# Optimization experiments

Hardware: AMD Instinct MI355X
Metric: run time of the kernel (lower is better)

The kernel has to match this reference:

```python
import jax, jax.numpy as jnp
import numpy as np

ALPHA = 2.0  # init kwarg alpha


def _edt(mask):
    """Exact Euclidean distance from each pixel to the nearest False pixel.
    mask: (H, W) bool. Matches scipy.ndimage.distance_transform_edt(mask).
    Separable algorithm: 1D L1 pass along columns, then exact min over columns.
    """
    H, W = mask.shape
    INF = jnp.float32(H + W)
    g0 = jnp.where(mask, INF, 0.0).astype(jnp.float32)  # 0 at background pixels

    def step(carry, row):
        g = jnp.minimum(row, carry + 1.0)
        return g, g

    _, fwd = jax.lax.scan(step, jnp.full((W,), INF, jnp.float32), g0)
    _, bwd = jax.lax.scan(step, jnp.full((W,), INF, jnp.float32), fwd[::-1])
    g = bwd[::-1]  # (H, W): vertical distance to nearest bg in same column

    j = jnp.arange(W, dtype=jnp.float32)
    d2 = (j[:, None] - j[None, :]) ** 2  # (Wj, Wk)
    # dist2[i, j] = min_k g[i, k]^2 + (j - k)^2   -> exact squared EDT
    dist2 = jnp.min(g[:, None, :] ** 2 + d2[None, :, :], axis=-1)  # (H, W)
    return jnp.sqrt(dist2)


def _distance_field(img):
    """img: (N, H, W) float. Replicates LogHausdorffDTLoss.distance_field per slice."""

    def one(ch):
        mask = ch > 0.5
        valid = jnp.logical_and(mask.any(), ~mask.all())
        field = _edt(mask) + _edt(~mask)  # fg_dist + bg_dist
        return jnp.where(valid, field, 0.0)

    # sequential map keeps peak memory to one (H, W, W) intermediate at a time
    return jax.lax.map(one, img)


def setup_inputs() -> dict:
    key = jax.random.key(0)
    k1, k2, k3 = jax.random.split(key, 3)
    B, C, H, W = 8, 4, 256, 256
    preds_S = jax.random.normal(k1, (B, C, H, W), dtype=jnp.float32)
    preds_T = jax.random.normal(k2, (B, C, H, W), dtype=jnp.float32)
    target = jax.random.uniform(k3, (B, 1, H, W), dtype=jnp.float32)
    return {"preds_S": preds_S, "preds_T": preds_T, "target": target}


def reference(preds_S, preds_T, target):
    # shapes already match -> no interpolation; sigmoid=False, softmax=True, C>1
    C = preds_S.shape[1]
    p = jax.nn.softmax(preds_S, axis=1)

    # to_onehot_y=True: target is overwritten by onehot(argmax(teacher)) (detached)
    pT = jax.lax.stop_gradient(preds_T)
    labels = jnp.argmax(pT, axis=1)  # (B, H, W)
    tgt = jax.nn.one_hot(labels, C, axis=1, dtype=p.dtype)  # (B, C, H, W)

    # include_background=False: drop channel 0
    p = p[:, 1:]
    tgt = tgt[:, 1:]
    B, Cc, H, W = p.shape

    pred_dt = _distance_field(jax.lax.stop_gradient(p).reshape(-1, H, W)).reshape(B, Cc, H, W)
    tgt_dt = _distance_field(tgt.reshape(-1, H, W)).reshape(B, Cc, H, W)
    pred_dt = jax.lax.stop_gradient(pred_dt)
    tgt_dt = jax.lax.stop_gradient(tgt_dt)

    err = (p - tgt) ** 2
    dist = pred_dt ** ALPHA + tgt_dt ** ALPHA
    # per-channel means all cover B*H*W elements -> mean of means == global mean
    loss = jnp.mean(err * dist)
    return jnp.log(loss + 1.0)
```

## Files before the change

### kernel.cpp

```cpp
#include <hip/hip_runtime.h>
#include <math.h>

#define HWTOT 65536
#define WD 256
#define HT 256
#define NSL 24

static constexpr size_t OFF_CNT   = 0;
static constexpr size_t OFF_PART  = 256;
static constexpr size_t HDR_BYTES = 256 + 6144 * 4;
static constexpr size_t OFF_MASK  = 24832;
static constexpr size_t OFF_ERR   = OFF_MASK + (size_t)NSL * HWTOT;
static constexpr size_t OFF_G     = OFF_ERR + (size_t)NSL * HWTOT * 2;

__global__ __launch_bounds__(256) void k_mask(
    const float* __restrict__ pS, const float* __restrict__ pT,
    unsigned char* __restrict__ mask, _Float16* __restrict__ err,
    int* __restrict__ cnts)
{
    __shared__ int lc[6];
    if (threadIdx.x < 6) lc[threadIdx.x] = 0;
    __syncthreads();

    int t  = blockIdx.x * 256 + threadIdx.x;
    int b  = t >> 16;
    int hw = t & (HWTOT - 1);

    const float* ps = pS + (size_t)b * 4 * HWTOT + hw;
    float s0 = ps[0], s1 = ps[HWTOT], s2 = ps[2 * HWTOT], s3 = ps[3 * HWTOT];
    float mx = fmaxf(fmaxf(s0, s1), fmaxf(s2, s3));
    float e0 = expf(s0 - mx), e1 = expf(s1 - mx), e2 = expf(s2 - mx), e3 = expf(s3 - mx);
    float inv = 1.0f / (e0 + e1 + e2 + e3);

    const float* pt = pT + (size_t)b * 4 * HWTOT + hw;
    float t0 = pt[0], t1 = pt[HWTOT], t2 = pt[2 * HWTOT], t3 = pt[3 * HWTOT];
    int lab = 0; float bm = t0;
    if (t1 > bm) { bm = t1; lab = 1; }
    if (t2 > bm) { bm = t2; lab = 2; }
    if (t3 > bm) { bm = t3; lab = 3; }

    float pv[3] = { e1 * inv, e2 * inv, e3 * inv };
    #pragma unroll
    for (int cc = 0; cc < 3; ++cc) {
        int sl = b * 3 + cc;
        bool mp = pv[cc] > 0.5f;
        bool mt = (lab == cc + 1);
        mask[(size_t)sl * HWTOT + hw] = (unsigned char)((mp ? 1 : 0) | (mt ? 2 : 0));
        float tcv = mt ? 1.0f : 0.0f;
        float ev = (pv[cc] - tcv) * (pv[cc] - tcv);
        err[(size_t)sl * HWTOT + hw] = (_Float16)ev;
        unsigned long long balP = __ballot(mp);
        unsigned long long balT = __ballot(mt);
        if ((threadIdx.x & 63) == 0) {
            atomicAdd(&lc[cc],     (int)__popcll(balP));
            atomicAdd(&lc[3 + cc], (int)__popcll(balT));
        }
    }
    __syncthreads();
    if (threadIdx.x < 3) {
        atomicAdd(&cnts[b * 3 + threadIdx.x], lc[threadIdx.x]);
    } else if (threadIdx.x < 6) {
        atomicAdd(&cnts[24 + b * 3 + (threadIdx.x - 3)], lc[threadIdx.x]);
    }
}

__global__ __launch_bounds__(256) void k_vert(
    const unsigned char* __restrict__ mask, unsigned short* __restrict__ g)
{
    int s = blockIdx.x;
    int f = blockIdx.y;
    int w = threadIdx.x;
    int bit = f >> 1;
    int pol = f & 1;

    const unsigned char* m = mask + (size_t)s * HWTOT + w;
    unsigned short* go = g + ((size_t)f * NSL + s) * HWTOT + w;

    unsigned gp[128];
    int prev = 512;
    #pragma unroll
    for (int hb = 0; hb < 16; ++hb) {
        unsigned char mb[16];
        #pragma unroll
        for (int i = 0; i < 16; ++i) mb[i] = m[(hb * 16 + i) * WD];
        #pragma unroll
        for (int i = 0; i < 16; ++i) {
            int h = hb * 16 + i;
            int mv = (mb[i] >> bit) & 1;
            int gv = (mv == pol) ? 0 : min(prev + 1, 512);
            prev = gv;
            if ((h & 1) == 0) gp[h >> 1] = (unsigned)gv;
            else              gp[h >> 1] |= (unsigned)gv << 16;
        }
    }
    prev = 512;
    #pragma unroll
    for (int hb = 15; hb >= 0; --hb) {
        unsigned short outv[16];
        #pragma unroll
        for (int i = 15; i >= 0; --i) {
            int h = hb * 16 + i;
            unsigned pk = gp[h >> 1];
            int gf = (h & 1) ? (int)(pk >> 16) : (int)(pk & 0xffffu);
            int gv = min(gf, prev + 1);
            prev = gv;
            outv[i] = (unsigned short)gv;
        }
        #pragma unroll
        for (int i = 0; i < 16; ++i) go[(hb * 16 + i) * WD] = outv[i];
    }
}

__global__ __launch_bounds__(256) void k_row(
    const _Float16* __restrict__ err, const unsigned short* __restrict__ gAll,
    const int* __restrict__ cnts, float* __restrict__ partials)
{
    int h  = blockIdx.x;
    int s  = blockIdx.y;
    int jo = threadIdx.x;

    __shared__ float4 g2[768];
    __shared__ float  wred[4];

    const size_t fstride = (size_t)NSL * HWTOT;
    size_t rbase = (size_t)s * HWTOT + h * WD + jo;

    int a  = gAll[rbase];
    int bb = gAll[fstride + rbase];
    int c  = gAll[2 * fstride + rbase];
    int dd = gAll[3 * fstride + rbase];

    int cp = cnts[s];
    int ct = cnts[24 + s];
    bool validP = (cp > 0) && (cp < HWTOT);
    bool validT = (ct > 0) && (ct < HWTOT);
    bool selP = (a > 0);
    bool selT = (c > 0);

    int gsp = selP ? a : bb; if (!validP) gsp = 0;
    int gst = selT ? c : dd; if (!validT) gst = 0;

    float fa = (float)(a * a), fb = (float)(bb * bb);
    float fc = (float)(c * c), fd = (float)(dd * dd);
    g2[256 + jo] = make_float4(fa, fb, fc, fd);
    float4 inf4 = make_float4(1e30f, 1e30f, 1e30f, 1e30f);
    g2[jo] = inf4;
    g2[512 + jo] = inf4;

    int R = min(max(gsp, gst), 256);
    #pragma unroll
    for (int i = 1; i < 64; i <<= 1) R = max(R, __shfl_xor(R, i));

    float m1 = (float)(gsp * gsp);
    float m2 = (float)(gst * gst);
    __syncthreads();

    for (int d = 1; d < R; ++d) {
        float4 L = g2[256 + jo - d];
        float4 Rv = g2[256 + jo + d];
        float d2 = (float)(d * d);
        float c1 = fminf(selP ? L.x : L.y, selP ? Rv.x : Rv.y);
        float c2 = fminf(selT ? L.z : L.w, selT ? Rv.z : Rv.w);
        m1 = fminf(m1, c1 + d2);
        m2 = fminf(m2, c2 + d2);
    }

    float contrib = (float)err[rbase] * (m1 + m2);

    #pragma unroll
    for (int off = 32; off > 0; off >>= 1) contrib += __shfl_down(contrib, off);
    if ((jo & 63) == 0) wred[jo >> 6] = contrib;
    __syncthreads();
    if (jo == 0) partials[s * 256 + h] = wred[0] + wred[1] + wred[2] + wred[3];
}

__global__ __launch_bounds__(256) void k_final(
    const float* __restrict__ partials, float* __restrict__ out)
{
    __shared__ double red[256];
    int t = threadIdx.x;
    double acc = 0.0;
    for (int i = t; i < NSL * 256; i += 256) acc += (double)partials[i];
    red[t] = acc;
    __syncthreads();
    for (int off = 128; off > 0; off >>= 1) {
        if (t < off) red[t] += red[t + off];
        __syncthreads();
    }
    if (t == 0) {
        double loss = red[0] / (double)((size_t)NSL * HWTOT);
        out[0] = (float)log(loss + 1.0);
    }
}

extern "C" void kernel_launch(void* const* d_in, const int* in_sizes, int n_in,
                              void* d_out, int out_size, void* d_ws, size_t ws_size,
                              hipStream_t stream)
{
    const float* pS = (const float*)d_in[0];
    const float* pT = (const float*)d_in[1];
    float* out = (float*)d_out;

    char* ws = (char*)d_ws;
    int*            cnts  = (int*)(ws + OFF_CNT);
    float*          parts = (float*)(ws + OFF_PART);
    unsigned char*  mask  = (unsigned char*)(ws + OFF_MASK);
    _Float16*       err   = (_Float16*)(ws + OFF_ERR);
    unsigned short* gAll  = (unsigned short*)(ws + OFF_G);

    hipMemsetAsync(ws, 0, HDR_BYTES, stream);

    k_mask <<<dim3(2048),     dim3(256), 0, stream>>>(pS, pT, mask, err, cnts);
    k_vert <<<dim3(NSL, 4),   dim3(256), 0, stream>>>(mask, gAll);
    k_row  <<<dim3(256, NSL), dim3(256), 0, stream>>>(err, gAll, cnts, parts);
    k_final<<<dim3(1),        dim3(256), 0, stream>>>(parts, out);
}
```

Before: 130.2 us.

## Compute combined boundary distance in one vertical pass and drop memset/atomics

```diff
diff --git a/kernel.cpp b/kernel.cpp
--- a/kernel.cpp
+++ b/kernel.cpp
@@ -6,25 +6,26 @@
 #define HT 256
 #define NSL 24
 
-static constexpr size_t OFF_CNT   = 0;
-static constexpr size_t OFF_PART  = 256;
-static constexpr size_t HDR_BYTES = 256 + 6144 * 4;
-static constexpr size_t OFF_MASK  = 24832;
-static constexpr size_t OFF_ERR   = OFF_MASK + (size_t)NSL * HWTOT;
-static constexpr size_t OFF_G     = OFF_ERR + (size_t)NSL * HWTOT * 2;
+static constexpr size_t OFF_CNT  = 0;
+static constexpr size_t OFF_PART = 256;
+static constexpr size_t OFF_PCNT = 24832;
+static constexpr size_t OFF_MASK = 49408;
+static constexpr size_t OFF_ERR  = OFF_MASK + (size_t)NSL * HWTOT;
+static constexpr size_t OFF_G    = OFF_ERR + (size_t)NSL * HWTOT * 2;
 
 __global__ __launch_bounds__(256) void k_mask(
     const float* __restrict__ pS, const float* __restrict__ pT,
     unsigned char* __restrict__ mask, _Float16* __restrict__ err,
-    int* __restrict__ cnts)
+    unsigned short* __restrict__ pcnt)
 {
     __shared__ int lc[6];
     if (threadIdx.x < 6) lc[threadIdx.x] = 0;
     __syncthreads();
 
-    int t  = blockIdx.x * 256 + threadIdx.x;
-    int b  = t >> 16;
-    int hw = t & (HWTOT - 1);
+    int blk = blockIdx.x;
+    int b   = blk >> 8;
+    int lb  = blk & 255;
+    int hw  = lb * 256 + threadIdx.x;
 
     const float* ps = pS + (size_t)b * 4 * HWTOT + hw;
     float s0 = ps[0], s1 = ps[HWTOT], s2 = ps[2 * HWTOT], s3 = ps[3 * HWTOT];
@@ -58,61 +59,75 @@
     }
     __syncthreads();
     if (threadIdx.x < 3) {
-        atomicAdd(&cnts[b * 3 + threadIdx.x], lc[threadIdx.x]);
+        int sl = b * 3 + threadIdx.x;
+        pcnt[(size_t)sl * 256 + lb] = (unsigned short)lc[threadIdx.x];
     } else if (threadIdx.x < 6) {
-        atomicAdd(&cnts[24 + b * 3 + (threadIdx.x - 3)], lc[threadIdx.x]);
-    }
-}
-
-__global__ __launch_bounds__(256) void k_vert(
-    const unsigned char* __restrict__ mask, unsigned short* __restrict__ g)
+        int sl = b * 3 + (threadIdx.x - 3);
+        pcnt[(size_t)(NSL + sl) * 256 + lb] = (unsigned short)lc[threadIdx.x];
+    }
+}
+
+__global__ __launch_bounds__(256, 1) void k_vert(
+    const unsigned char* __restrict__ mask, const unsigned short* __restrict__ pcnt,
+    unsigned short* __restrict__ g, int* __restrict__ cnts)
 {
     int s = blockIdx.x;
     int f = blockIdx.y;
     int w = threadIdx.x;
-    int bit = f >> 1;
-    int pol = f & 1;
 
     const unsigned char* m = mask + (size_t)s * HWTOT + w;
     unsigned short* go = g + ((size_t)f * NSL + s) * HWTOT + w;
 
-    unsigned gp[128];
-    int prev = 512;
+    unsigned up[128];
+    unsigned mb32[8];
+    int prevm = -1, d = 512;
     #pragma unroll
     for (int hb = 0; hb < 16; ++hb) {
-        unsigned char mb[16];
-        #pragma unroll
-        for (int i = 0; i < 16; ++i) mb[i] = m[(hb * 16 + i) * WD];
+        unsigned char mraw[16];
+        #pragma unroll
+        for (int i = 0; i < 16; ++i) mraw[i] = m[(hb * 16 + i) * WD];
         #pragma unroll
         for (int i = 0; i < 16; ++i) {
             int h = hb * 16 + i;
-            int mv = (mb[i] >> bit) & 1;
-            int gv = (mv == pol) ? 0 : min(prev + 1, 512);
-            prev = gv;
-            if ((h & 1) == 0) gp[h >> 1] = (unsigned)gv;
-            else              gp[h >> 1] |= (unsigned)gv << 16;
+            int mv = (mraw[i] >> f) & 1;
+            d = (prevm < 0) ? 512 : ((mv != prevm) ? 1 : min(d + 1, 512));
+            prevm = mv;
+            if (h & 1) up[h >> 1] |= (unsigned)d << 16;
+            else       up[h >> 1]  = (unsigned)d;
+            if ((h & 31) == 0) mb32[h >> 5]  = (unsigned)mv;
+            else               mb32[h >> 5] |= (unsigned)mv << (h & 31);
         }
     }
-    prev = 512;
+    int nextm = -1; d = 512;
     #pragma unroll
     for (int hb = 15; hb >= 0; --hb) {
         unsigned short outv[16];
         #pragma unroll
         for (int i = 15; i >= 0; --i) {
             int h = hb * 16 + i;
-            unsigned pk = gp[h >> 1];
-            int gf = (h & 1) ? (int)(pk >> 16) : (int)(pk & 0xffffu);
-            int gv = min(gf, prev + 1);
-            prev = gv;
-            outv[i] = (unsigned short)gv;
+            int mv = (mb32[h >> 5] >> (h & 31)) & 1;
+            d = (nextm < 0) ? 512 : ((mv != nextm) ? 1 : min(d + 1, 512));
+            nextm = mv;
+            unsigned pk = up[h >> 1];
+            int du = (h & 1) ? (int)(pk >> 16) : (int)(pk & 0xffffu);
+            outv[i] = (unsigned short)min(du, d);
         }
         #pragma unroll
         for (int i = 0; i < 16; ++i) go[(hb * 16 + i) * WD] = outv[i];
     }
+
+    __shared__ int cr[4];
+    int v = (int)pcnt[((size_t)f * NSL + s) * 256 + w];
+    #pragma unroll
+    for (int i = 1; i < 64; i <<= 1) v += __shfl_xor(v, i);
+    if ((w & 63) == 0) cr[w >> 6] = v;
+    __syncthreads();
+    if (w == 0) cnts[f * NSL + s] = cr[0] + cr[1] + cr[2] + cr[3];
 }
 
 __global__ __launch_bounds__(256) void k_row(
     const _Float16* __restrict__ err, const unsigned short* __restrict__ gAll,
+    const unsigned char* __restrict__ mask,
     const int* __restrict__ cnts, float* __restrict__ partials)
 {
     int h  = blockIdx.x;
@@ -125,28 +140,27 @@
     const size_t fstride = (size_t)NSL * HWTOT;
     size_t rbase = (size_t)s * HWTOT + h * WD + jo;
 
-    int a  = gAll[rbase];
-    int bb = gAll[fstride + rbase];
-    int c  = gAll[2 * fstride + rbase];
-    int dd = gAll[3 * fstride + rbase];
+    int gcP = gAll[rbase];
+    int gcT = gAll[fstride + rbase];
+    int mb  = mask[rbase];
+    bool selP = mb & 1;
+    bool selT = (mb >> 1) & 1;
 
     int cp = cnts[s];
-    int ct = cnts[24 + s];
+    int ct = cnts[NSL + s];
     bool validP = (cp > 0) && (cp < HWTOT);
     bool validT = (ct > 0) && (ct < HWTOT);
-    bool selP = (a > 0);
-    bool selT = (c > 0);
-
-    int gsp = selP ? a : bb; if (!validP) gsp = 0;
-    int gst = selT ? c : dd; if (!validT) gst = 0;
-
-    float fa = (float)(a * a), fb = (float)(bb * bb);
-    float fc = (float)(c * c), fd = (float)(dd * dd);
-    g2[256 + jo] = make_float4(fa, fb, fc, fd);
+
+    float fP = (float)(gcP * gcP);
+    float fT = (float)(gcT * gcT);
+    g2[256 + jo] = make_float4(selP ? fP : 0.0f, selP ? 0.0f : fP,
+                               selT ? fT : 0.0f, selT ? 0.0f : fT);
     float4 inf4 = make_float4(1e30f, 1e30f, 1e30f, 1e30f);
     g2[jo] = inf4;
     g2[512 + jo] = inf4;
 
+    int gsp = validP ? gcP : 0;
+    int gst = validT ? gcT : 0;
     int R = min(max(gsp, gst), 256);
     #pragma unroll
     for (int i = 1; i < 64; i <<= 1) R = max(R, __shfl_xor(R, i));
@@ -155,10 +169,10 @@
     float m2 = (float)(gst * gst);
     __syncthreads();
 
-    for (int d = 1; d < R; ++d) {
-        float4 L = g2[256 + jo - d];
-        float4 Rv = g2[256 + jo + d];
-        float d2 = (float)(d * d);
+    for (int dd = 1; dd < R; ++dd) {
+        float4 L  = g2[256 + jo - dd];
+        float4 Rv = g2[256 + jo + dd];
+        float d2 = (float)(dd * dd);
         float c1 = fminf(selP ? L.x : L.y, selP ? Rv.x : Rv.y);
         float c2 = fminf(selT ? L.z : L.w, selT ? Rv.z : Rv.w);
         m1 = fminf(m1, c1 + d2);
@@ -204,14 +218,13 @@
     char* ws = (char*)d_ws;
     int*            cnts  = (int*)(ws + OFF_CNT);
     float*          parts = (float*)(ws + OFF_PART);
+    unsigned short* pcnt  = (unsigned short*)(ws + OFF_PCNT);
     unsigned char*  mask  = (unsigned char*)(ws + OFF_MASK);
     _Float16*       err   = (_Float16*)(ws + OFF_ERR);
     unsigned short* gAll  = (unsigned short*)(ws + OFF_G);
 
-    hipMemsetAsync(ws, 0, HDR_BYTES, stream);
-
-    k_mask <<<dim3(2048),     dim3(256), 0, stream>>>(pS, pT, mask, err, cnts);
-    k_vert <<<dim3(NSL, 4),   dim3(256), 0, stream>>>(mask, gAll);
-    k_row  <<<dim3(256, NSL), dim3(256), 0, stream>>>(err, gAll, cnts, parts);
+    k_mask <<<dim3(2048),     dim3(256), 0, stream>>>(pS, pT, mask, err, pcnt);
+    k_vert <<<dim3(NSL, 2),   dim3(256), 0, stream>>>(mask, pcnt, gAll, cnts);
+    k_row  <<<dim3(256, NSL), dim3(256), 0, stream>>>(err, gAll, mask, cnts, parts);
     k_final<<<dim3(1),        dim3(256), 0, stream>>>(parts, out);
 }
```

Measured after the change: 112.5 us. 1.16x faster.
